# Performance work log

Measured on AMD Instinct MI355X. Metric: run time of the kernel, lower is better.

The kernel has to match this reference:

```python
import jax, jax.numpy as jnp
import numpy as np

N = 4194304          # flat pixel batch (~2 full 1080p frames)
NUM_CAMERAS = 8
NUM_FRAMES = 1000
EPS = 1e-6


def setup_inputs() -> dict:
    key = jax.random.key(0)
    ks = jax.random.split(key, 8)
    W, H = 1920, 1080
    exposure_params = 0.2 * jax.random.normal(ks[0], (NUM_FRAMES,), jnp.float32)
    vignetting_params = 0.05 * jax.random.normal(ks[1], (NUM_CAMERAS, 3, 5), jnp.float32)
    color_params = 0.05 * jax.random.normal(ks[2], (NUM_FRAMES, 8), jnp.float32)
    # CRF raw init matching the module: softplus-inverse of 1.0 with minima (0.3,0.3,0.1), offset 0
    def _sp_inv(x, m):
        return float(np.log(np.expm1(max(1e-5, x - m))))
    crf0 = jnp.array([_sp_inv(1.0, 0.3), _sp_inv(1.0, 0.3), _sp_inv(1.0, 0.1), 0.0], jnp.float32)
    crf_params = (jnp.broadcast_to(crf0, (NUM_CAMERAS, 3, 4))
                  + 0.05 * jax.random.normal(ks[3], (NUM_CAMERAS, 3, 4), jnp.float32))
    rgb = jax.random.uniform(ks[4], (N, 3), jnp.float32)
    pixel_coords = jax.random.uniform(ks[5], (N, 2), jnp.float32) * jnp.array([W, H], jnp.float32)
    camera_idcs = jax.random.randint(ks[6], (N,), 0, NUM_CAMERAS, jnp.int32)
    frame_idcs = jax.random.randint(ks[7], (N,), 0, NUM_FRAMES, jnp.int32)
    return dict(exposure_params=exposure_params, vignetting_params=vignetting_params,
                color_params=color_params, crf_params=crf_params, rgb=rgb,
                pixel_coords=pixel_coords, camera_idcs=camera_idcs, frame_idcs=frame_idcs,
                resolution_w=W, resolution_h=H)


def _ppisp(exposure_params, vignetting_params, color_params, crf_params,
           rgb, pixel_coords, camera_idcs, frame_idcs, resolution_w, resolution_h):
    # 1) per-frame exposure (EV scale)
    exp_scale = jnp.exp2(exposure_params[frame_idcs])[:, None]            # [N,1]
    x = rgb * exp_scale                                                    # [N,3]

    # 2) per-camera, per-channel radial vignetting: params = [cx, cy, a1, a2, a3]
    vig = vignetting_params[camera_idcs]                                   # [N,3,5]
    u = pixel_coords[:, 0] / jnp.float32(resolution_w) - 0.5               # [N]
    v = pixel_coords[:, 1] / jnp.float32(resolution_h) - 0.5               # [N]
    du = u[:, None] - vig[..., 0]                                          # [N,3]
    dv = v[:, None] - vig[..., 1]
    r2 = du * du + dv * dv                                                 # [N,3]
    falloff = 1.0 + r2 * (vig[..., 2] + r2 * (vig[..., 3] + r2 * vig[..., 4]))
    x = x * falloff

    # 3) per-frame color: WB gains (r,b) + off-diagonal 3x3 mixing matrix (8 params)
    cp = color_params[frame_idcs]                                          # [N,8]
    gains = jnp.stack([jnp.exp(cp[:, 0]), jnp.ones_like(cp[:, 0]), jnp.exp(cp[:, 1])], axis=-1)
    x = x * gains
    one = jnp.ones_like(cp[:, 0])
    M = jnp.stack([
        jnp.stack([one,      cp[:, 2], cp[:, 3]], axis=-1),
        jnp.stack([cp[:, 4], one,      cp[:, 5]], axis=-1),
        jnp.stack([cp[:, 6], cp[:, 7], one     ], axis=-1)], axis=-2)      # [N,3,3]
    x = jnp.einsum('nij,nj->ni', M, x)

    # 4) per-camera, per-channel 4-param sigmoid CRF, identity at init
    crf = crf_params[camera_idcs]                                          # [N,3,4]
    a = jax.nn.softplus(crf[..., 0]) + 0.3
    b = jax.nn.softplus(crf[..., 1]) + 0.3
    c = jax.nn.softplus(crf[..., 2]) + 0.1
    d = crf[..., 3]
    xc = jnp.clip(x, EPS, 1.0)
    xa = xc ** a
    out = xa / (xa + (c * (1.0 - xc) + EPS) ** b) + d                      # [N,3]
    return out


def reference(exposure_params, vignetting_params, color_params, crf_params,
              rgb, pixel_coords, camera_idcs, frame_idcs, resolution_w, resolution_h):
    return _ppisp(exposure_params, vignetting_params, color_params, crf_params,
                  rgb, pixel_coords, camera_idcs, frame_idcs, resolution_w, resolution_h)
```

## Files before the change

kernel.cpp:

```cpp
#include <hip/hip_runtime.h>


#define FREC 5
#define CREC 5

__global__ void ppisp_precompute(const float* __restrict__ expo,
                                 const float* __restrict__ colorp,
                                 const float* __restrict__ vigp,
                                 const float* __restrict__ crfp,
                                 float* __restrict__ ftab,
                                 float* __restrict__ camtab,
                                 int num_frames) {
    int tid = blockIdx.x * blockDim.x + threadIdx.x;
    if (tid < num_frames) {
        float e = exp2f(expo[tid]);
        const float* cp = colorp + tid * 8;
        float* f = ftab + tid * 10;
        f[0] = e * expf(cp[0]);
        f[1] = e;
        f[2] = e * expf(cp[1]);
        f[3] = cp[2];
        f[4] = cp[3];
        f[5] = cp[4];
        f[6] = cp[5];
        f[7] = cp[6];
        f[8] = cp[7];
        f[9] = 0.f;
    }
    if (tid < 24) {
        const float* vp = vigp + tid * 5;
        const float* cf = crfp + tid * 4;
        float* r = camtab + tid * 10;
        r[0] = vp[0];
        r[1] = vp[1];
        r[2] = vp[2];
        r[3] = vp[3];
        r[4] = vp[4];
        r[5] = log1pf(expf(cf[0])) + 0.3f;
        r[6] = log1pf(expf(cf[1])) + 0.3f;
        r[7] = log1pf(expf(cf[2])) + 0.1f;
        r[8] = cf[3];
        r[9] = 0.f;
    }
}

__global__ __launch_bounds__(256) void ppisp_main(
    const float4* __restrict__ rgb4,
    const float4* __restrict__ pc4,
    const int4*   __restrict__ cam4,
    const int4*   __restrict__ frm4,
    const float2* __restrict__ ftab2,
    const float2* __restrict__ camtab2,
    const int*    __restrict__ resw,
    const int*    __restrict__ resh,
    float4* __restrict__ out4,
    int ngroups, int groups_per_block, int num_frames) {
    __shared__ float2 sft[5000];
    __shared__ float2 scam[120];

    int tid = threadIdx.x;
    int nf2 = num_frames * FREC;
    for (int i = tid; i < nf2; i += 256) sft[i] = ftab2[i];
    if (tid < 120) scam[tid] = camtab2[tid];
    __syncthreads();

    float invW = 1.0f / (float)resw[0];
    float invH = 1.0f / (float)resh[0];

    int gbase = blockIdx.x * groups_per_block;
    int gend = gbase + groups_per_block;
    if (gend > ngroups) gend = ngroups;

    for (int g = gbase + tid; g < gend; g += 256) {
        float4 r0  = rgb4[(size_t)g * 3 + 0];
        float4 r1  = rgb4[(size_t)g * 3 + 1];
        float4 r2v = rgb4[(size_t)g * 3 + 2];
        float4 p0  = pc4[(size_t)g * 2 + 0];
        float4 p1  = pc4[(size_t)g * 2 + 1];
        int4 cams = cam4[g];
        int4 frms = frm4[g];

        float rgb[4][3] = {{r0.x, r0.y, r0.z},
                           {r0.w, r1.x, r1.y},
                           {r1.z, r1.w, r2v.x},
                           {r2v.y, r2v.z, r2v.w}};
        float px[4] = {p0.x, p0.z, p1.x, p1.z};
        float py[4] = {p0.y, p0.w, p1.y, p1.w};
        int camA[4] = {cams.x, cams.y, cams.z, cams.w};
        int frmA[4] = {frms.x, frms.y, frms.z, frms.w};

        float o[12];

#pragma unroll
        for (int p = 0; p < 4; ++p) {
            int fb = frmA[p] * FREC;
            float2 F0 = sft[fb + 0];
            float2 F1 = sft[fb + 1];
            float2 F2 = sft[fb + 2];
            float2 F3 = sft[fb + 3];
            float2 F4 = sft[fb + 4];
            float g3[3] = {F0.x, F0.y, F1.x};

            float u = px[p] * invW - 0.5f;
            float v = py[p] * invH - 0.5f;

            float x[3], av[3], bv[3], cv[3], dv2[3];
#pragma unroll
            for (int ch = 0; ch < 3; ++ch) {
                int cb = (camA[p] * 3 + ch) * CREC;
                float2 C0 = scam[cb + 0];
                float2 C1 = scam[cb + 1];
                float2 C2 = scam[cb + 2];
                float2 C3 = scam[cb + 3];
                float2 C4 = scam[cb + 4];
                float du = u - C0.x;
                float dv = v - C0.y;
                float r2 = du * du + dv * dv;
                float fall = 1.0f + r2 * (C1.x + r2 * (C1.y + r2 * C2.x));
                x[ch] = rgb[p][ch] * g3[ch] * fall;
                av[ch] = C2.y; bv[ch] = C3.x; cv[ch] = C3.y; dv2[ch] = C4.x;
            }

            float y0 = x[0] + F1.y * x[1] + F2.x * x[2];
            float y1 = F2.y * x[0] + x[1] + F3.x * x[2];
            float y2 = F3.y * x[0] + F4.x * x[1] + x[2];
            float yv[3] = {y0, y1, y2};

#pragma unroll
            for (int ch = 0; ch < 3; ++ch) {
                float xc = fminf(fmaxf(yv[ch], 1e-6f), 1.0f);
                float la = __builtin_amdgcn_logf(xc);
                float xa = __builtin_amdgcn_exp2f(av[ch] * la);
                float t  = cv[ch] * (1.0f - xc) + 1e-6f;
                float tb = __builtin_amdgcn_exp2f(bv[ch] * __builtin_amdgcn_logf(t));
                o[p * 3 + ch] = xa * __builtin_amdgcn_rcpf(xa + tb) + dv2[ch];
            }
        }

        out4[(size_t)g * 3 + 0] = make_float4(o[0], o[1], o[2], o[3]);
        out4[(size_t)g * 3 + 1] = make_float4(o[4], o[5], o[6], o[7]);
        out4[(size_t)g * 3 + 2] = make_float4(o[8], o[9], o[10], o[11]);
    }
}

extern "C" void kernel_launch(void* const* d_in, const int* in_sizes, int n_in,
                              void* d_out, int out_size, void* d_ws, size_t ws_size,
                              hipStream_t stream) {
    const float* expo   = (const float*)d_in[0];
    const float* vigp   = (const float*)d_in[1];
    const float* colorp = (const float*)d_in[2];
    const float* crfp   = (const float*)d_in[3];
    const float* rgb    = (const float*)d_in[4];
    const float* pc     = (const float*)d_in[5];
    const int*   cam    = (const int*)d_in[6];
    const int*   frm    = (const int*)d_in[7];
    const int*   rw     = (const int*)d_in[8];
    const int*   rh     = (const int*)d_in[9];

    int num_frames = in_sizes[0];
    int N = in_sizes[4] / 3;

    float* ftab = (float*)d_ws;
    size_t ftab_bytes = ((size_t)num_frames * 10 * sizeof(float) + 255) & ~(size_t)255;
    float* camtab = (float*)((char*)d_ws + ftab_bytes);

    int pre_threads = 256;
    int pre_blocks = (num_frames + pre_threads - 1) / pre_threads;
    if (pre_blocks < 1) pre_blocks = 1;
    ppisp_precompute<<<pre_blocks, pre_threads, 0, stream>>>(
        expo, colorp, vigp, crfp, ftab, camtab, num_frames);

    int ngroups = N / 4;
    int blocks = 2048;
    int groups_per_block = (ngroups + blocks - 1) / blocks;
    ppisp_main<<<blocks, 256, 0, stream>>>(
        (const float4*)rgb, (const float4*)pc, (const int4*)cam, (const int4*)frm,
        (const float2*)ftab, (const float2*)camtab, rw, rh, (float4*)d_out,
        ngroups, groups_per_block, num_frames);
}
```

Before: 186.1 us.

## Pack per-frame table as bf16 and use float4 camera table to cut LDS footprint

Per-frame gains and color-matrix entries are stored as packed bf16 pairs (24 bytes per frame instead of 40), which shrinks the shared-memory table from 40KB to 24KB. The per-camera table is reorganized into float4 rows so each camera's parameters load with seven 128-bit LDS reads. Launch bounds request 5 blocks per SM, and the grid drops to 1536 blocks so more blocks can be resident at once. Storing the parameters in bf16 loses precision in the gains and matrix terms, which may exceed the accuracy tolerance.

```diff
diff --git a/kernel.cpp b/kernel.cpp
--- a/kernel.cpp
+++ b/kernel.cpp
@@ -1,36 +1,42 @@
 #include <hip/hip_runtime.h>
 
 
-#define FREC 5
-#define CREC 5
+__device__ __forceinline__ unsigned bf16r(float x) {
+    unsigned b = __float_as_uint(x);
+    return (b + 0x7fffu + ((b >> 16) & 1u)) >> 16;
+}
+__device__ __forceinline__ unsigned packbf(float lo, float hi) {
+    return bf16r(lo) | (bf16r(hi) << 16);
+}
+__device__ __forceinline__ float ulo(unsigned u) { return __uint_as_float(u << 16); }
+__device__ __forceinline__ float uhi(unsigned u) { return __uint_as_float(u & 0xffff0000u); }
 
 __global__ void ppisp_precompute(const float* __restrict__ expo,
                                  const float* __restrict__ colorp,
                                  const float* __restrict__ vigp,
                                  const float* __restrict__ crfp,
-                                 float* __restrict__ ftab,
+                                 unsigned* __restrict__ ftab,
                                  float* __restrict__ camtab,
-                                 int num_frames) {
+                                 int num_frames, int ncam) {
     int tid = blockIdx.x * blockDim.x + threadIdx.x;
     if (tid < num_frames) {
         float e = exp2f(expo[tid]);
         const float* cp = colorp + tid * 8;
-        float* f = ftab + tid * 10;
-        f[0] = e * expf(cp[0]);
-        f[1] = e;
-        f[2] = e * expf(cp[1]);
-        f[3] = cp[2];
-        f[4] = cp[3];
-        f[5] = cp[4];
-        f[6] = cp[5];
-        f[7] = cp[6];
-        f[8] = cp[7];
-        f[9] = 0.f;
+        float g_r = e * expf(cp[0]);
+        float g_b = e * expf(cp[1]);
+        unsigned* f = ftab + tid * 6;
+        f[0] = packbf(g_r, e);
+        f[1] = packbf(g_b, cp[2]);
+        f[2] = packbf(cp[3], cp[4]);
+        f[3] = packbf(cp[5], cp[6]);
+        f[4] = packbf(cp[7], 0.f);
+        f[5] = 0u;
     }
-    if (tid < 24) {
+    if (tid < ncam * 3) {
+        int c = tid / 3, ch = tid % 3;
         const float* vp = vigp + tid * 5;
         const float* cf = crfp + tid * 4;
-        float* r = camtab + tid * 10;
+        float* r = camtab + c * 28 + ch * 9;
         r[0] = vp[0];
         r[1] = vp[1];
         r[2] = vp[2];
@@ -40,28 +46,28 @@
         r[6] = log1pf(expf(cf[1])) + 0.3f;
         r[7] = log1pf(expf(cf[2])) + 0.1f;
         r[8] = cf[3];
-        r[9] = 0.f;
+        if (ch == 0) camtab[c * 28 + 27] = 0.f;
     }
 }
 
-__global__ __launch_bounds__(256) void ppisp_main(
+__global__ __launch_bounds__(256, 5) void ppisp_main(
     const float4* __restrict__ rgb4,
     const float4* __restrict__ pc4,
     const int4*   __restrict__ cam4,
     const int4*   __restrict__ frm4,
-    const float2* __restrict__ ftab2,
-    const float2* __restrict__ camtab2,
+    const uint2*  __restrict__ ftab2,
+    const float4* __restrict__ camtab4,
     const int*    __restrict__ resw,
     const int*    __restrict__ resh,
     float4* __restrict__ out4,
-    int ngroups, int groups_per_block, int num_frames) {
-    __shared__ float2 sft[5000];
-    __shared__ float2 scam[120];
+    int ngroups, int groups_per_block, int num_frames, int ncam) {
+    __shared__ uint2  sft[3000];
+    __shared__ float4 scam[56];
 
     int tid = threadIdx.x;
-    int nf2 = num_frames * FREC;
-    for (int i = tid; i < nf2; i += 256) sft[i] = ftab2[i];
-    if (tid < 120) scam[tid] = camtab2[tid];
+    int nfw = num_frames * 3;
+    for (int i = tid; i < nfw; i += 256) sft[i] = ftab2[i];
+    if (tid < ncam * 7) scam[tid] = camtab4[tid];
     __syncthreads();
 
     float invW = 1.0f / (float)resw[0];
@@ -80,12 +86,14 @@
         int4 cams = cam4[g];
         int4 frms = frm4[g];
 
-        float rgb[4][3] = {{r0.x, r0.y, r0.z},
-                           {r0.w, r1.x, r1.y},
-                           {r1.z, r1.w, r2v.x},
-                           {r2v.y, r2v.z, r2v.w}};
+        float rgbp[4][3] = {{r0.x, r0.y, r0.z},
+                            {r0.w, r1.x, r1.y},
+                            {r1.z, r1.w, r2v.x},
+                            {r2v.y, r2v.z, r2v.w}};
         float px[4] = {p0.x, p0.z, p1.x, p1.z};
-        float py[4] = {p0.y, p0.w, p1.y, p1.w};
+        float py[4] = {p0.y, p0.w, p1.y, p1.z};
+        py[2] = p1.y; py[3] = p1.w;
+        py[0] = p0.y; py[1] = p0.w;
         int camA[4] = {cams.x, cams.y, cams.z, cams.w};
         int frmA[4] = {frms.x, frms.y, frms.z, frms.w};
 
@@ -93,48 +101,68 @@
 
 #pragma unroll
         for (int p = 0; p < 4; ++p) {
-            int fb = frmA[p] * FREC;
-            float2 F0 = sft[fb + 0];
-            float2 F1 = sft[fb + 1];
-            float2 F2 = sft[fb + 2];
-            float2 F3 = sft[fb + 3];
-            float2 F4 = sft[fb + 4];
-            float g3[3] = {F0.x, F0.y, F1.x};
+            int fb = frmA[p] * 3;
+            uint2 A = sft[fb + 0];
+            uint2 B = sft[fb + 1];
+            unsigned Cw = sft[fb + 2].x;
+            float g_r = ulo(A.x), g_g = uhi(A.x), g_b = ulo(A.y);
+            float m01 = uhi(A.y), m02 = ulo(B.x), m10 = uhi(B.x);
+            float m12 = ulo(B.y), m20 = uhi(B.y), m21 = ulo(Cw);
+
+            int cb = camA[p] * 7;
+            float4 q0 = scam[cb + 0];
+            float4 q1 = scam[cb + 1];
+            float4 q2 = scam[cb + 2];
+            float4 q3 = scam[cb + 3];
+            float4 q4 = scam[cb + 4];
+            float4 q5 = scam[cb + 5];
+            float4 q6 = scam[cb + 6];
 
             float u = px[p] * invW - 0.5f;
             float v = py[p] * invH - 0.5f;
 
-            float x[3], av[3], bv[3], cv[3], dv2[3];
-#pragma unroll
-            for (int ch = 0; ch < 3; ++ch) {
-                int cb = (camA[p] * 3 + ch) * CREC;
-                float2 C0 = scam[cb + 0];
-                float2 C1 = scam[cb + 1];
-                float2 C2 = scam[cb + 2];
-                float2 C3 = scam[cb + 3];
-                float2 C4 = scam[cb + 4];
-                float du = u - C0.x;
-                float dv = v - C0.y;
-                float r2 = du * du + dv * dv;
-                float fall = 1.0f + r2 * (C1.x + r2 * (C1.y + r2 * C2.x));
-                x[ch] = rgb[p][ch] * g3[ch] * fall;
-                av[ch] = C2.y; bv[ch] = C3.x; cv[ch] = C3.y; dv2[ch] = C4.x;
-            }
-
-            float y0 = x[0] + F1.y * x[1] + F2.x * x[2];
-            float y1 = F2.y * x[0] + x[1] + F3.x * x[2];
-            float y2 = F3.y * x[0] + F4.x * x[1] + x[2];
-            float yv[3] = {y0, y1, y2};
-
-#pragma unroll
-            for (int ch = 0; ch < 3; ++ch) {
-                float xc = fminf(fmaxf(yv[ch], 1e-6f), 1.0f);
-                float la = __builtin_amdgcn_logf(xc);
-                float xa = __builtin_amdgcn_exp2f(av[ch] * la);
-                float t  = cv[ch] * (1.0f - xc) + 1e-6f;
-                float tb = __builtin_amdgcn_exp2f(bv[ch] * __builtin_amdgcn_logf(t));
-                o[p * 3 + ch] = xa * __builtin_amdgcn_rcpf(xa + tb) + dv2[ch];
-            }
+            float cx0 = q0.x, cy0 = q0.y, a10 = q0.z, a20 = q0.w, a30 = q1.x;
+            float aa0 = q1.y, bb0 = q1.z, cc0 = q1.w, dd0 = q2.x;
+            float cx1 = q2.y, cy1 = q2.z, a11 = q2.w, a21 = q3.x, a31 = q3.y;
+            float aa1 = q3.z, bb1 = q3.w, cc1 = q4.x, dd1 = q4.y;
+            float cx2 = q4.z, cy2 = q4.w, a12 = q5.x, a22 = q5.y, a32 = q5.z;
+            float aa2 = q5.w, bb2 = q6.x, cc2 = q6.y, dd2 = q6.z;
+
+            float du0 = u - cx0, dv0 = v - cy0;
+            float du1 = u - cx1, dv1 = v - cy1;
+            float du2 = u - cx2, dv2 = v - cy2;
+            float r20 = du0 * du0 + dv0 * dv0;
+            float r21 = du1 * du1 + dv1 * dv1;
+            float r22 = du2 * du2 + dv2 * dv2;
+            float fa0 = 1.0f + r20 * (a10 + r20 * (a20 + r20 * a30));
+            float fa1 = 1.0f + r21 * (a11 + r21 * (a21 + r21 * a31));
+            float fa2 = 1.0f + r22 * (a12 + r22 * (a22 + r22 * a32));
+
+            float x0 = rgbp[p][0] * g_r * fa0;
+            float x1 = rgbp[p][1] * g_g * fa1;
+            float x2 = rgbp[p][2] * g_b * fa2;
+
+            float y0 = x0 + m01 * x1 + m02 * x2;
+            float y1 = m10 * x0 + x1 + m12 * x2;
+            float y2 = m20 * x0 + m21 * x1 + x2;
+
+            float xc0 = fminf(fmaxf(y0, 1e-6f), 1.0f);
+            float xc1 = fminf(fmaxf(y1, 1e-6f), 1.0f);
+            float xc2 = fminf(fmaxf(y2, 1e-6f), 1.0f);
+
+            float xa0 = __builtin_amdgcn_exp2f(aa0 * __builtin_amdgcn_logf(xc0));
+            float xa1 = __builtin_amdgcn_exp2f(aa1 * __builtin_amdgcn_logf(xc1));
+            float xa2 = __builtin_amdgcn_exp2f(aa2 * __builtin_amdgcn_logf(xc2));
+            float t0 = cc0 * (1.0f - xc0) + 1e-6f;
+            float t1 = cc1 * (1.0f - xc1) + 1e-6f;
+            float t2 = cc2 * (1.0f - xc2) + 1e-6f;
+            float tb0 = __builtin_amdgcn_exp2f(bb0 * __builtin_amdgcn_logf(t0));
+            float tb1 = __builtin_amdgcn_exp2f(bb1 * __builtin_amdgcn_logf(t1));
+            float tb2 = __builtin_amdgcn_exp2f(bb2 * __builtin_amdgcn_logf(t2));
+
+            o[p * 3 + 0] = xa0 * __builtin_amdgcn_rcpf(xa0 + tb0) + dd0;
+            o[p * 3 + 1] = xa1 * __builtin_amdgcn_rcpf(xa1 + tb1) + dd1;
+            o[p * 3 + 2] = xa2 * __builtin_amdgcn_rcpf(xa2 + tb2) + dd2;
         }
 
         out4[(size_t)g * 3 + 0] = make_float4(o[0], o[1], o[2], o[3]);
@@ -158,23 +186,24 @@
     const int*   rh     = (const int*)d_in[9];
 
     int num_frames = in_sizes[0];
+    int ncam = in_sizes[1] / 15;
     int N = in_sizes[4] / 3;
 
-    float* ftab = (float*)d_ws;
-    size_t ftab_bytes = ((size_t)num_frames * 10 * sizeof(float) + 255) & ~(size_t)255;
+    unsigned* ftab = (unsigned*)d_ws;
+    size_t ftab_bytes = ((size_t)num_frames * 6 * sizeof(unsigned) + 255) & ~(size_t)255;
     float* camtab = (float*)((char*)d_ws + ftab_bytes);
 
     int pre_threads = 256;
     int pre_blocks = (num_frames + pre_threads - 1) / pre_threads;
     if (pre_blocks < 1) pre_blocks = 1;
     ppisp_precompute<<<pre_blocks, pre_threads, 0, stream>>>(
-        expo, colorp, vigp, crfp, ftab, camtab, num_frames);
+        expo, colorp, vigp, crfp, ftab, camtab, num_frames, ncam);
 
     int ngroups = N / 4;
-    int blocks = 2048;
+    int blocks = 1536;
     int groups_per_block = (ngroups + blocks - 1) / blocks;
     ppisp_main<<<blocks, 256, 0, stream>>>(
         (const float4*)rgb, (const float4*)pc, (const int4*)cam, (const int4*)frm,
-        (const float2*)ftab, (const float2*)camtab, rw, rh, (float4*)d_out,
-        ngroups, groups_per_block, num_frames);
-}
+        (const uint2*)ftab, (const float4*)camtab, rw, rh, (float4*)d_out,
+        ngroups, groups_per_block, num_frames, ncam);
+}
```

After: 182.6 us. About the same (-1.9%).
